# Optimization experiments

Hardware: AMD Instinct MI355X
Metric: run time of the kernel (lower is better)

Reference implementation:

```python
import jax, jax.numpy as jnp
import numpy as np

K = 4          # temporal_depth
IN_SIZE = 1024 # conv input channels
DN = ('NCDHW', 'OIDHW', 'NCDHW')


def setup_inputs() -> dict:
    key = jax.random.key(0)
    ks = jax.random.split(key, 12)
    B, T, C, H, W = 1, 8, IN_SIZE, 14, 14
    s = 0.02
    return {
        'videos': jax.random.normal(ks[0], (B, T, C, H, W), dtype=jnp.float32),
        # Conv3d(in_size, in_size, 3, padding='same')
        'conv1_w': jax.random.normal(ks[1], (IN_SIZE, IN_SIZE, 3, 3, 3), dtype=jnp.float32) * s,
        'conv1_b': jax.random.normal(ks[2], (IN_SIZE,), dtype=jnp.float32) * s,
        # Conv3d(in_size, 512, 3, padding='same')
        'conv2_w': jax.random.normal(ks[3], (512, IN_SIZE, 3, 3, 3), dtype=jnp.float32) * s,
        'conv2_b': jax.random.normal(ks[4], (512,), dtype=jnp.float32) * s,
        # Linear(512,512) -> Linear(512,512) -> Linear(512,128), torch (out,in) layout
        'l1_w': jax.random.normal(ks[5], (512, 512), dtype=jnp.float32) * s,
        'l1_b': jax.random.normal(ks[6], (512,), dtype=jnp.float32) * s,
        'l2_w': jax.random.normal(ks[7], (512, 512), dtype=jnp.float32) * s,
        'l2_b': jax.random.normal(ks[8], (512,), dtype=jnp.float32) * s,
        'l3_w': jax.random.normal(ks[9], (128, 512), dtype=jnp.float32) * s,
        'l3_b': jax.random.normal(ks[10], (128,), dtype=jnp.float32) * s,
    }


def reference(videos, conv1_w, conv1_b, conv2_w, conv2_b,
              l1_w, l1_b, l2_w, l2_b, l3_w, l3_b):
    B, T, C, H, W = videos.shape
    # prepend k zero frames, as in the torch code
    padded = jnp.concatenate(
        [jnp.zeros((B, K, C, H, W), videos.dtype), videos], axis=1)
    # window o covers padded frames [o, o+K) -> strictly-past original frames
    idx = jnp.arange(T)[:, None] + jnp.arange(K)[None, :]      # (T, K)
    win = padded[:, idx]                                        # (B, T, K, C, H, W)
    # permute(1,0,2,3): channels first, depth=K -> batch all windows together
    win = win.transpose(0, 1, 3, 2, 4, 5).reshape(B * T, C, K, H, W)
    # Conv3d + ReLU + Conv3d + ReLU, each with 'same' zero padding per window
    h = jax.lax.conv_general_dilated(win, conv1_w, (1, 1, 1), 'SAME',
                                     dimension_numbers=DN)
    h = jax.nn.relu(h + conv1_b[None, :, None, None, None])
    h = jax.lax.conv_general_dilated(h, conv2_w, (1, 1, 1), 'SAME',
                                     dimension_numbers=DN)
    h = jax.nn.relu(h + conv2_b[None, :, None, None, None])
    # MaxPool3d over the full (D,H,W) extent == global max per channel
    pooled = jnp.max(h, axis=(2, 3, 4))                         # (B*T, 512)
    x = jax.nn.relu(pooled @ l1_w.T + l1_b)
    x = jax.nn.relu(x @ l2_w.T + l2_b)
    x = jax.nn.relu(x @ l3_w.T + l3_b)                          # (B*T, 128)
    return x.reshape(B, T, 128)
```

## Files before the change

### kernel.cpp

```cpp
#include <hip/hip_runtime.h>

typedef __attribute__((ext_vector_type(8))) short short8;
typedef __attribute__((ext_vector_type(4))) int int4v;
typedef __attribute__((ext_vector_type(4))) float floatx4;
typedef __attribute__((ext_vector_type(4))) unsigned short ushort4v;

#define DEV __device__ __forceinline__

constexpr int M_TOT = 6272;
constexpr int M_PAD = 6400;

DEV void async_ld16(const void* g, void* l) {
  __builtin_amdgcn_global_load_lds(
      (const __attribute__((address_space(1))) unsigned int*)g,
      (__attribute__((address_space(3))) unsigned int*)l,
      16, 0, 0);
}

DEV unsigned short f2bf(float x) {
  union { float f; unsigned int u; } v; v.f = x;
  unsigned int u = v.u;
  u += 0x7FFFu + ((u >> 16) & 1u);
  return (unsigned short)(u >> 16);
}

DEV float bf2f(unsigned short s) {
  union { unsigned int u; float f; } v; v.u = ((unsigned int)s) << 16;
  return v.f;
}

__global__ void wtrans(const float* __restrict__ w, unsigned short* __restrict__ wt,
                       int total ) {
  __shared__ unsigned short l[256 * 27];
  const int tid  = threadIdx.x;
  const int base = blockIdx.x * 256;
  #pragma unroll 1
  for (int j = tid; j < 256 * 27; j += 256)
    l[j] = f2bf(w[(size_t)base * 27 + j]);
  __syncthreads();
  #pragma unroll 1
  for (int tap = 0; tap < 27; ++tap)
    wt[(size_t)tap * total + base + tid] = l[tid * 27 + tap];
}

__global__ void build_P1(const float* __restrict__ videos, unsigned short* __restrict__ P1) {
  const int f  = blockIdx.x;
  const int c0 = blockIdx.y * 64;
  const int tid = threadIdx.x;
  __shared__ unsigned short tile[64][196];

  #pragma unroll 1
  for (int it = 0; it < 49; ++it) {
    int idx = it * 256 + tid;
    int c = idx / 196, r = idx - c * 196;
    tile[c][r] = f2bf(videos[(size_t)(f * 1024 + c0 + c) * 196 + r]);
  }
  __syncthreads();

  const int c   = tid & 63;
  const int hwq = tid >> 6;
  #pragma unroll 1
  for (int s = 1; s <= 4; ++s) {
    int t = f + 5 - s;
    if (t > 7) continue;
    unsigned short* dst = P1 + (size_t)(t * 6 + s) * 256 * 1024 + (size_t)c0;
    #pragma unroll 1
    for (int it = 0; it < 49; ++it) {
      int hw = it * 4 + hwq;
      int h = hw / 14, w = hw - h * 14;
      dst[(size_t)((h + 1) * 16 + (w + 1)) * 1024 + c] = tile[c][hw];
    }
  }
}

#define DSR(dst, addr, off) \
  asm volatile("ds_read_b128 %0, %1 offset:" #off : "=&v"(dst) : "v"(addr))
#define WAITL(n) \
  asm volatile("s_waitcnt lgkmcnt(" #n ")" ::: "memory"); \
  __builtin_amdgcn_sched_barrier(0)
#define SB0 __builtin_amdgcn_sched_barrier(0)

template <int COUT, bool TCOND>
__global__ __launch_bounds__(512, 2) void conv_gemm(
    const unsigned short* __restrict__ P,
    const unsigned short* __restrict__ Wt,
    const unsigned int* __restrict__ sched,
    unsigned short* __restrict__ part)
{
  constexpr int CIN = 1024;
  __shared__ short lA[4][8192];
  __shared__ short lB[4][8192];
  const int tid  = threadIdx.x;
  const int wave = tid >> 6;
  const int lane = tid & 63;

  const unsigned int e = sched[blockIdx.x];
  const int x2   = e & 31;
  const int nidx = (e >> 5) & 3;
  const int zs   = (e >> 7) & 7;
  const int tap0 = (e >> 10) & 31;
  const int tap1 = (e >> 15) & 31;
  const int m0 = x2 * 256;
  const int n0 = nidx * 256;
  unsigned short* partOut = part + (size_t)zs * M_PAD * COUT;

  bool kdv[3] = {false, false, false};
  {
    const int cA = m0 / 196;
    int cB = (m0 + 255) / 196; if (cB > 31) cB = 31;
    for (int c = cA; c <= cB; ++c) {
      int t = c >> 2, d = c & 3;
      #pragma unroll
      for (int kd = 0; kd < 3; ++kd) {
        int s = d + kd;
        bool ok = (s >= 1) && (s <= 4);
        if (TCOND) ok = ok && (s >= 5 - t);
        kdv[kd] = kdv[kd] || ok;
      }
    }
  }

  const int arow = tid >> 2;
  const int aswz = (((tid & 3) ^ ((arow >> 1) & 3)) << 4);
  int aG[2], bG[2];
  #pragma unroll
  for (int q = 0; q < 2; ++q) {
    int m = m0 + q * 128 + arow;
    int t = m / 784;  int r2 = m - t * 784;
    int d = r2 / 196; int r3 = r2 - d * 196;
    int h = r3 / 14;  int w = r3 - h * 14;
    aG[q] = ((((t * 6 + d) * 16 + h) * 16 + w) * CIN) * 2 + aswz;
    bG[q] = (n0 + q * 128 + arow) * (CIN * 2) + aswz;
  }

  int nvt = 0;
  for (int tp = tap0; tp < tap1; ++tp) if (kdv[tp / 9]) ++nvt;
  const int steps = nvt * 32;
  int tap_s = tap0;
  while (tap_s < tap1 && !kdv[tap_s / 9]) ++tap_s;
  int c_s = 0;
  int stA = 0, stB = 0;
  auto setBases = [&]() {
    const int kd = tap_s / 9, rm = tap_s - kd * 9;
    const int kh = rm / 3, kw = rm - kh * 3;
    stA = ((((kd * 16) + kh) * 16 + kw) * CIN) * 2 + c_s * 2;
    stB = tap_s * (COUT * CIN * 2) + c_s * 2;
  };
  auto adv = [&]() {
    c_s += 32;
    if (c_s == CIN) { c_s = 0; do { ++tap_s; } while (tap_s < tap1 && !kdv[tap_s / 9]); }
  };

  const char* Pb = (const char*)P;
  const char* Wb = (const char*)Wt;
  char* lAc = (char*)&lA[0][0];
  char* lBc = (char*)&lB[0][0];
  const unsigned ldsA0 =
      (unsigned)(size_t)(__attribute__((address_space(3))) char*)lAc;
  const unsigned ldsB0 =
      (unsigned)(size_t)(__attribute__((address_space(3))) char*)lBc;

  #pragma unroll 1
  for (int s = 0; s < 3; ++s) {
    setBases();
    char* dA = lAc + s * 16384;
    char* dB = lBc + s * 16384;
    async_ld16(Pb + aG[0] + stA, dA + tid * 16);
    async_ld16(Wb + bG[0] + stB, dB + tid * 16);
    async_ld16(Pb + aG[1] + stA, dA + 8192 + tid * 16);
    async_ld16(Wb + bG[1] + stB, dB + 8192 + tid * 16);
    adv();
  }
  asm volatile("s_waitcnt vmcnt(4)" ::: "memory");
  __builtin_amdgcn_s_barrier();
  SB0;

  const int wm   = (wave >> 2) * 128;
  const int wn   = (wave & 3) * 64;
  const int quad = lane >> 4;
  const int l15  = lane & 15;
  const int segc = ((quad ^ ((l15 >> 1) & 3)) << 4);
  const unsigned rowA = ((unsigned)(wm + l15) << 6) + segc;
  const unsigned rowB = ((unsigned)(wn + l15) << 6) + segc;

  floatx4 acc[8][4];
  const floatx4 zero4 = {0.f, 0.f, 0.f, 0.f};
  #pragma unroll
  for (int i = 0; i < 8; ++i)
    #pragma unroll
    for (int j = 0; j < 4; ++j) acc[i][j] = zero4;

  int4v pbE0, pbE1, pbE2, pbE3, paE0, paE1;
  int4v pbO0, pbO1, pbO2, pbO3, paO0, paO1;

  {
    const unsigned aB = ldsA0 + rowA;
    const unsigned bB = ldsB0 + rowB;
    DSR(pbE0, bB, 0);
    DSR(pbE1, bB, 1024);
    DSR(pbE2, bB, 2048);
    DSR(pbE3, bB, 3072);
    DSR(paE0, aB, 0);
    DSR(paE1, aB, 1024);
  }
  SB0;

#define MFMA_GRP(ACCI, AV)                                                  \
  {                                                                         \
    short8 a_ = __builtin_bit_cast(short8, AV);                             \
    acc[ACCI][0] = __builtin_amdgcn_mfma_f32_16x16x32_bf16(a_, bs0, acc[ACCI][0], 0, 0, 0); \
    acc[ACCI][1] = __builtin_amdgcn_mfma_f32_16x16x32_bf16(a_, bs1, acc[ACCI][1], 0, 0, 0); \
    acc[ACCI][2] = __builtin_amdgcn_mfma_f32_16x16x32_bf16(a_, bs2, acc[ACCI][2], 0, 0, 0); \
    acc[ACCI][3] = __builtin_amdgcn_mfma_f32_16x16x32_bf16(a_, bs3, acc[ACCI][3], 0, 0, 0); \
  }

#define STEP_BODY(U, PB0, PB1, PB2, PB3, PA0, PA1, NB0, NB1, NB2, NB3, NA0, NA1) \
  {                                                                         \
    const int u_ = (U);                                                     \
    const bool h3s = (u_ + 3 < steps);                                      \
    const unsigned aB = ldsA0 + (unsigned)(u_ & 3) * 16384u + rowA;         \
    int4v f2, f3, f4, f5, f6, f7;                                           \
    DSR(f2, aB, 2048);                                                      \
    DSR(f3, aB, 3072);                                                      \
    DSR(f4, aB, 4096);                                                      \
    DSR(f5, aB, 5120);                                                      \
    DSR(f6, aB, 6144);                                                      \
    DSR(f7, aB, 7168);                                                      \
    SB0;                                                                    \
    if (h3s) {                                                              \
      setBases();                                                           \
      char* dA = lAc + ((u_ + 3) & 3) * 16384;                              \
      char* dB = lBc + ((u_ + 3) & 3) * 16384;                              \
      async_ld16(Pb + aG[0] + stA, dA + tid * 16);                          \
      async_ld16(Wb + bG[0] + stB, dB + tid * 16);                          \
      async_ld16(Pb + aG[1] + stA, dA + 8192 + tid * 16);                   \
      async_ld16(Wb + bG[1] + stB, dB + 8192 + tid * 16);                   \
      adv();                                                                \
    }                                                                       \
    SB0;                                                                    \
    __builtin_amdgcn_s_setprio(1);                                          \
    short8 bs0, bs1, bs2, bs3;                                              \
    WAITL(7);                                                               \
    bs0 = __builtin_bit_cast(short8, PB0);                                  \
    bs1 = __builtin_bit_cast(short8, PB1);                                  \
    bs2 = __builtin_bit_cast(short8, PB2);                                  \
    bs3 = __builtin_bit_cast(short8, PB3);                                  \
    MFMA_GRP(0, PA0);                                                       \
    WAITL(6); MFMA_GRP(1, PA1);                                             \
    WAITL(5); MFMA_GRP(2, f2);                                              \
    WAITL(4); MFMA_GRP(3, f3);                                              \
    WAITL(3); MFMA_GRP(4, f4);                                              \
    WAITL(2); MFMA_GRP(5, f5);                                              \
    WAITL(1); MFMA_GRP(6, f6);                                              \
    WAITL(0); MFMA_GRP(7, f7);                                              \
    __builtin_amdgcn_s_setprio(0);                                          \
    SB0;                                                                    \
    if (u_ + 1 < steps) {                                                   \
      const unsigned nA = ldsA0 + (unsigned)((u_ + 1) & 3) * 16384u + rowA; \
      const unsigned nB = ldsB0 + (unsigned)((u_ + 1) & 3) * 16384u + rowB; \
      DSR(NB0, nB, 0);                                                      \
      DSR(NB1, nB, 1024);                                                   \
      DSR(NB2, nB, 2048);                                                   \
      DSR(NB3, nB, 3072);                                                   \
      DSR(NA0, nA, 0);                                                      \
      DSR(NA1, nA, 1024);                                                   \
    }                                                                       \
    SB0;                                                                    \
    if (h3s) { asm volatile("s_waitcnt vmcnt(4)" ::: "memory"); }           \
    else     { asm volatile("s_waitcnt vmcnt(0)" ::: "memory"); }           \
    SB0;                                                                    \
    __builtin_amdgcn_s_barrier();                                           \
    SB0;                                                                    \
  }

  #pragma unroll 1
  for (int t = 0; t < steps; t += 2) {
    STEP_BODY(t,     pbE0, pbE1, pbE2, pbE3, paE0, paE1,
                     pbO0, pbO1, pbO2, pbO3, paO0, paO1);
    STEP_BODY(t + 1, pbO0, pbO1, pbO2, pbO3, paO0, paO1,
                     pbE0, pbE1, pbE2, pbE3, paE0, paE1);
  }

  asm volatile("s_waitcnt vmcnt(0) lgkmcnt(0)" ::: "memory");
  __builtin_amdgcn_s_barrier();

  #pragma unroll
  for (int j = 0; j < 4; ++j) {
    const int o = n0 + wn + j * 16 + l15;
    #pragma unroll
    for (int i = 0; i < 8; ++i) {
      #pragma unroll
      for (int r = 0; r < 4; ++r) {
        int m = m0 + wm + i * 16 + quad * 4 + r;
        partOut[(size_t)m * COUT + o] = f2bf(acc[i][j][r]);
      }
    }
  }
#undef STEP_BODY
#undef MFMA_GRP
}

__global__ void reduce_conv1(const unsigned short* __restrict__ part,
                             const float* __restrict__ bias,
                             unsigned short* __restrict__ P2) {
  const int idx = blockIdx.x * 256 + threadIdx.x;
  const int m  = idx >> 8;
  const int o4 = (idx & 255) * 4;
  const size_t ss = (size_t)M_PAD * 1024;
  const size_t base = (size_t)m * 1024 + o4;
  ushort4v p0 = *(const ushort4v*)(part + base);
  ushort4v p1 = *(const ushort4v*)(part + ss + base);
  ushort4v p2 = *(const ushort4v*)(part + 2 * ss + base);
  ushort4v out;
  #pragma unroll
  for (int k = 0; k < 4; ++k) {
    float v = bf2f(p0[k]) + bf2f(p1[k]) + bf2f(p2[k]) + bias[o4 + k];
    out[k] = f2bf(v > 0.f ? v : 0.f);
  }
  int t = m / 784;  int r2 = m - t * 784;
  int d = r2 / 196; int r3 = r2 - d * 196;
  int h = r3 / 14;  int w = r3 - h * 14;
  size_t didx = (size_t)(((t * 6 + d + 1) * 16 + (h + 1)) * 16 + (w + 1)) * 1024 + o4;
  *(ushort4v*)(P2 + didx) = out;
}

__global__ void reduce_conv2(const unsigned short* __restrict__ part,
                             const float* __restrict__ bias,
                             unsigned short* __restrict__ h2) {
  const int idx = blockIdx.x * 256 + threadIdx.x;
  const int m  = idx >> 7;
  const int o4 = (idx & 127) * 4;
  const size_t base = (size_t)m * 512 + o4;
  const size_t ss = (size_t)M_PAD * 512;
  float acc[4];
  #pragma unroll
  for (int k = 0; k < 4; ++k) acc[k] = bias[o4 + k];
  #pragma unroll
  for (int s = 0; s < 5; ++s) {
    ushort4v p = *(const ushort4v*)(part + (size_t)s * ss + base);
    #pragma unroll
    for (int k = 0; k < 4; ++k) acc[k] += bf2f(p[k]);
  }
  ushort4v out;
  #pragma unroll
  for (int k = 0; k < 4; ++k) out[k] = f2bf(acc[k] > 0.f ? acc[k] : 0.f);
  *(ushort4v*)(h2 + base) = out;
}

__global__ void pool1(const unsigned short* __restrict__ h2,
                      unsigned short* __restrict__ partial) {
  const int t = blockIdx.x / 28, ch = blockIdx.x % 28, o = threadIdx.x;
  const unsigned short* src = h2 + ((size_t)t * 784 + ch * 28) * 512 + o;
  unsigned short m = 0;
  #pragma unroll 4
  for (int i = 0; i < 28; ++i) { unsigned short v = src[(size_t)i * 512]; m = v > m ? v : m; }
  partial[((size_t)t * 28 + ch) * 512 + o] = m;
}

__global__ void pool2(const unsigned short* __restrict__ partial, float* __restrict__ pooled) {
  const int t = blockIdx.x, o = threadIdx.x;
  const unsigned short* src = partial + (size_t)t * 28 * 512 + o;
  unsigned short m = 0;
  #pragma unroll 4
  for (int i = 0; i < 28; ++i) { unsigned short v = src[(size_t)i * 512]; m = v > m ? v : m; }
  pooled[t * 512 + o] = bf2f(m);
}

__global__ void mlp_kernel(const float* __restrict__ pooled,
                           const float* __restrict__ w1, const float* __restrict__ b1,
                           const float* __restrict__ w2, const float* __restrict__ b2,
                           const float* __restrict__ w3, const float* __restrict__ b3,
                           float* __restrict__ out) {
  const int t = blockIdx.x, j = threadIdx.x;
  __shared__ float xa[512], xb[512];
  xa[j] = pooled[t * 512 + j];
  __syncthreads();
  {
    const float4* wr = (const float4*)(w1 + (size_t)j * 512);
    float s = b1[j];
    #pragma unroll 4
    for (int k = 0; k < 128; ++k) {
      float4 wv = wr[k];
      s += wv.x * xa[4*k] + wv.y * xa[4*k+1] + wv.z * xa[4*k+2] + wv.w * xa[4*k+3];
    }
    xb[j] = fmaxf(s, 0.f);
  }
  __syncthreads();
  {
    const float4* wr = (const float4*)(w2 + (size_t)j * 512);
    float s = b2[j];
    #pragma unroll 4
    for (int k = 0; k < 128; ++k) {
      float4 wv = wr[k];
      s += wv.x * xb[4*k] + wv.y * xb[4*k+1] + wv.z * xb[4*k+2] + wv.w * xb[4*k+3];
    }
    xa[j] = fmaxf(s, 0.f);
  }
  __syncthreads();
  if (j < 128) {
    const float4* wr = (const float4*)(w3 + (size_t)j * 512);
    float s = b3[j];
    #pragma unroll 4
    for (int k = 0; k < 128; ++k) {
      float4 wv = wr[k];
      s += wv.x * xa[4*k] + wv.y * xa[4*k+1] + wv.z * xa[4*k+2] + wv.w * xa[4*k+3];
    }
    out[t * 128 + j] = fmaxf(s, 0.f);
  }
}

static int build_sched(bool conv1, unsigned int* out) {
  const int nt = conv1 ? 4 : 2;
  unsigned int L[256];
  int cnt = 0;
  for (int n = 0; n < nt; ++n) {
    for (int x2 = 0; x2 < 25; ++x2) {
      const int m0 = x2 * 256;
      bool kdv[3] = {false, false, false};
      const int cA = m0 / 196;
      int cB = (m0 + 255) / 196; if (cB > 31) cB = 31;
      for (int c = cA; c <= cB; ++c) {
        int t = c >> 2, d = c & 3;
        for (int kd = 0; kd < 3; ++kd) {
          int s = d + kd;
          bool ok = (s >= 1 && s <= 4);
          if (conv1) ok = ok && (s >= 5 - t);
          kdv[kd] = kdv[kd] || ok;
        }
      }
      int vt[27], nv = 0;
      for (int tp = 0; tp < 27; ++tp) if (kdv[tp / 9]) vt[nv++] = tp;
      if (!nv) continue;
      const int ns = conv1 ? (nv / 9) : ((nv == 27) ? 5 : 4);
      for (int s = 0; s < ns; ++s) {
        int b0 = nv * s / ns, b1 = nv * (s + 1) / ns;
        int tp0 = vt[b0], tp1 = vt[b1 - 1] + 1;
        L[cnt++] = (unsigned int)(x2 | (n << 5) | (s << 7) | (tp0 << 10) | (tp1 << 15));
      }
    }
  }
  const int q = cnt / 8, r = cnt % 8;
  int pos = 0;
  for (int b = 0; b < 8; ++b) {
    const int nb = q + (b < r ? 1 : 0);
    for (int j = 0; j < nb; ++j) out[j * 8 + b] = L[pos++];
  }
  return cnt;
}

extern "C" void kernel_launch(void* const* d_in, const int* in_sizes, int n_in,
                              void* d_out, int out_size, void* d_ws, size_t ws_size,
                              hipStream_t stream) {
  const float* videos = (const float*)d_in[0];
  const float* c1w = (const float*)d_in[1];
  const float* c1b = (const float*)d_in[2];
  const float* c2w = (const float*)d_in[3];
  const float* c2b = (const float*)d_in[4];
  const float* l1w = (const float*)d_in[5];
  const float* l1b = (const float*)d_in[6];
  const float* l2w = (const float*)d_in[7];
  const float* l2b = (const float*)d_in[8];
  const float* l3w = (const float*)d_in[9];
  const float* l3b = (const float*)d_in[10];

  char* ws = (char*)d_ws;
  unsigned short* P12   = (unsigned short*)(ws);
  unsigned short* W1t   = (unsigned short*)(ws + 26738688);
  unsigned short* W2t   = (unsigned short*)(ws + 26738688);
  unsigned short* h2    = (unsigned short*)(ws + 55050240);
  float*          pooled= (float*)(ws + 61472768);
  unsigned short* ppart = (unsigned short*)(ws + 61489152);
  unsigned short* part  = (unsigned short*)(ws + 83361792);
  unsigned int* dsched1 = (unsigned int*)(ws + 122683392);
  unsigned int* dsched2 = (unsigned int*)(ws + 122684416);
  float* out = (float*)d_out;

  static unsigned int s1h[256], s2h[256];
  const int n1 = build_sched(true,  s1h);
  const int n2 = build_sched(false, s2h);
  hipMemcpyAsync(dsched1, s1h, sizeof(s1h), hipMemcpyHostToDevice, stream);
  hipMemcpyAsync(dsched2, s2h, sizeof(s2h), hipMemcpyHostToDevice, stream);

  hipMemsetAsync(ws, 0, 26738688, stream);
  hipMemsetAsync(part, 0, 39321600, stream);

  wtrans<<<4096, 256, 0, stream>>>(c1w, W1t, 1024 * 1024);
  build_P1<<<dim3(8, 16), 256, 0, stream>>>(videos, P12);

  conv_gemm<1024, true ><<<n1, 512, 0, stream>>>(P12, W1t, dsched1, part);

  wtrans<<<2048, 256, 0, stream>>>(c2w, W2t, 512 * 1024);
  reduce_conv1<<<6272, 256, 0, stream>>>(part, c1b, P12);
  hipMemsetAsync((char*)part + 32505856, 0, 262144, stream);

  conv_gemm<512, false><<<n2, 512, 0, stream>>>(P12, W2t, dsched2, part);
  reduce_conv2<<<3136, 256, 0, stream>>>(part, c2b, h2);

  pool1<<<224, 512, 0, stream>>>(h2, ppart);
  pool2<<<8, 512, 0, stream>>>(ppart, pooled);
  mlp_kernel<<<8, 512, 0, stream>>>(pooled, l1w, l1b, l2w, l2b, l3w, l3b, out);
}
```

Baseline: 748.0 us.

## Bake schedules into constant memory, drop memsets, fuse pool2 into MLP, simplify addressing

Schedules are computed at compile time into __constant__ tables, which removes two host-to-device copies and the host-side build each call. The 39MB zeroing of the partial buffer is dropped, and the reduce kernels now read only the split count that actually exists for each row tile. pool2 is folded into the MLP kernel, and the GEMM load addressing switches from recomputing offsets to incrementing pointers. The risk is that padded rows or splits that were never written could be read if a count table is wrong.

```diff
diff --git a/kernel.cpp b/kernel.cpp
--- a/kernel.cpp
+++ b/kernel.cpp
@@ -28,6 +28,73 @@
   union { unsigned int u; float f; } v; v.u = ((unsigned int)s) << 16;
   return v.f;
 }
+
+struct Sched { unsigned v[256]; int n; };
+struct NsTab { unsigned char v[25]; };
+
+constexpr void cell_kdv(bool conv1, int x2, bool kdv[3]) {
+  const int m0 = x2 * 256;
+  const int cA = m0 / 196;
+  int cB = (m0 + 255) / 196; if (cB > 31) cB = 31;
+  for (int c = cA; c <= cB; ++c) {
+    int t = c >> 2, d = c & 3;
+    for (int kd = 0; kd < 3; ++kd) {
+      int s = d + kd;
+      bool ok = (s >= 1 && s <= 4);
+      if (conv1) ok = ok && (s >= 5 - t);
+      kdv[kd] = kdv[kd] || ok;
+    }
+  }
+}
+
+constexpr Sched mk_sched(bool conv1) {
+  Sched out{};
+  const int nt = conv1 ? 4 : 2;
+  unsigned L[256] = {};
+  int cnt = 0;
+  for (int n = 0; n < nt; ++n) {
+    for (int x2 = 0; x2 < 25; ++x2) {
+      bool kdv[3] = {false, false, false};
+      cell_kdv(conv1, x2, kdv);
+      int vt[27] = {}; int nv = 0;
+      for (int tp = 0; tp < 27; ++tp) if (kdv[tp / 9]) vt[nv++] = tp;
+      if (!nv) continue;
+      const int ns = conv1 ? (nv / 9) : ((nv == 27) ? 5 : 4);
+      for (int s = 0; s < ns; ++s) {
+        int b0 = nv * s / ns, b1 = nv * (s + 1) / ns;
+        int tp0 = vt[b0], tp1 = vt[b1 - 1] + 1;
+        L[cnt++] = (unsigned)(x2 | (n << 5) | (s << 7) | (tp0 << 10) | (tp1 << 15));
+      }
+    }
+  }
+  const int q = cnt / 8, r = cnt % 8;
+  int pos = 0;
+  for (int b = 0; b < 8; ++b) {
+    const int nb = q + (b < r ? 1 : 0);
+    for (int j = 0; j < nb; ++j) out.v[j * 8 + b] = L[pos++];
+  }
+  out.n = cnt;
+  return out;
+}
+
+constexpr NsTab mk_ns(bool conv1) {
+  NsTab t{};
+  for (int x2 = 0; x2 < 25; ++x2) {
+    bool kdv[3] = {false, false, false};
+    cell_kdv(conv1, x2, kdv);
+    int nv = 0;
+    for (int tp = 0; tp < 27; ++tp) if (kdv[tp / 9]) ++nv;
+    t.v[x2] = (nv == 0) ? 0 : (unsigned char)(conv1 ? (nv / 9) : ((nv == 27) ? 5 : 4));
+  }
+  return t;
+}
+
+constexpr Sched S1h = mk_sched(true);
+constexpr Sched S2h = mk_sched(false);
+__constant__ Sched dS1 = mk_sched(true);
+__constant__ Sched dS2 = mk_sched(false);
+__constant__ NsTab dNS1 = mk_ns(true);
+__constant__ NsTab dNS2 = mk_ns(false);
 
 __global__ void wtrans(const float* __restrict__ w, unsigned short* __restrict__ wt,
                        int total ) {
@@ -84,7 +151,6 @@
 __global__ __launch_bounds__(512, 2) void conv_gemm(
     const unsigned short* __restrict__ P,
     const unsigned short* __restrict__ Wt,
-    const unsigned int* __restrict__ sched,
     unsigned short* __restrict__ part)
 {
   constexpr int CIN = 1024;
@@ -94,7 +160,7 @@
   const int wave = tid >> 6;
   const int lane = tid & 63;
 
-  const unsigned int e = sched[blockIdx.x];
+  const unsigned int e = (TCOND ? dS1 : dS2).v[blockIdx.x];
   const int x2   = e & 31;
   const int nidx = (e >> 5) & 3;
   const int zs   = (e >> 7) & 7;
@@ -136,23 +202,32 @@
   int nvt = 0;
   for (int tp = tap0; tp < tap1; ++tp) if (kdv[tp / 9]) ++nvt;
   const int steps = nvt * 32;
-  int tap_s = tap0;
-  while (tap_s < tap1 && !kdv[tap_s / 9]) ++tap_s;
-  int c_s = 0;
-  int stA = 0, stB = 0;
-  auto setBases = [&]() {
-    const int kd = tap_s / 9, rm = tap_s - kd * 9;
-    const int kh = rm / 3, kw = rm - kh * 3;
-    stA = ((((kd * 16) + kh) * 16 + kw) * CIN) * 2 + c_s * 2;
-    stB = tap_s * (COUT * CIN * 2) + c_s * 2;
-  };
-  auto adv = [&]() {
-    c_s += 32;
-    if (c_s == CIN) { c_s = 0; do { ++tap_s; } while (tap_s < tap1 && !kdv[tap_s / 9]); }
-  };
-
   const char* Pb = (const char*)P;
   const char* Wb = (const char*)Wt;
+
+  int tapS = tap0;
+  while (tapS < tap1 && !kdv[tapS / 9]) ++tapS;
+  int scnt = 0;
+  const char *pa0 = nullptr, *pa1 = nullptr, *pb0 = nullptr, *pb1 = nullptr;
+  auto tapBase = [&]() {
+    const int kd = tapS / 9, rm = tapS - kd * 9;
+    const int kh = rm / 3, kw = rm - kh * 3;
+    const int tA = ((((kd * 16) + kh) * 16 + kw) * CIN) * 2;
+    const int tB = tapS * (COUT * CIN * 2);
+    pa0 = Pb + aG[0] + tA;  pa1 = Pb + aG[1] + tA;
+    pb0 = Wb + bG[0] + tB;  pb1 = Wb + bG[1] + tB;
+  };
+  auto advS = [&]() {
+    if (++scnt == 32) {
+      scnt = 0;
+      do { ++tapS; } while (tapS < tap1 && !kdv[tapS / 9]);
+      if (tapS < tap1) tapBase();
+    } else {
+      pa0 += 64; pa1 += 64; pb0 += 64; pb1 += 64;
+    }
+  };
+  tapBase();
+
   char* lAc = (char*)&lA[0][0];
   char* lBc = (char*)&lB[0][0];
   const unsigned ldsA0 =
@@ -162,14 +237,13 @@
 
   #pragma unroll 1
   for (int s = 0; s < 3; ++s) {
-    setBases();
     char* dA = lAc + s * 16384;
     char* dB = lBc + s * 16384;
-    async_ld16(Pb + aG[0] + stA, dA + tid * 16);
-    async_ld16(Wb + bG[0] + stB, dB + tid * 16);
-    async_ld16(Pb + aG[1] + stA, dA + 8192 + tid * 16);
-    async_ld16(Wb + bG[1] + stB, dB + 8192 + tid * 16);
-    adv();
+    async_ld16(pa0, dA + tid * 16);
+    async_ld16(pb0, dB + tid * 16);
+    async_ld16(pa1, dA + 8192 + tid * 16);
+    async_ld16(pb1, dB + 8192 + tid * 16);
+    advS();
   }
   asm volatile("s_waitcnt vmcnt(4)" ::: "memory");
   __builtin_amdgcn_s_barrier();
@@ -228,14 +302,13 @@
     DSR(f7, aB, 7168);                                                      \
     SB0;                                                                    \
     if (h3s) {                                                              \
-      setBases();                                                           \
       char* dA = lAc + ((u_ + 3) & 3) * 16384;                              \
       char* dB = lBc + ((u_ + 3) & 3) * 16384;                              \
-      async_ld16(Pb + aG[0] + stA, dA + tid * 16);                          \
-      async_ld16(Wb + bG[0] + stB, dB + tid * 16);                          \
-      async_ld16(Pb + aG[1] + stA, dA + 8192 + tid * 16);                   \
-      async_ld16(Wb + bG[1] + stB, dB + 8192 + tid * 16);                   \
-      adv();                                                                \
+      async_ld16(pa0, dA + tid * 16);                                       \
+      async_ld16(pb0, dB + tid * 16);                                       \
+      async_ld16(pa1, dA + 8192 + tid * 16);                                \
+      async_ld16(pb1, dB + 8192 + tid * 16);                                \
+      advS();                                                               \
     }                                                                       \
     SB0;                                                                    \
     __builtin_amdgcn_s_setprio(1);                                          \
@@ -303,20 +376,23 @@
 __global__ void reduce_conv1(const unsigned short* __restrict__ part,
                              const float* __restrict__ bias,
                              unsigned short* __restrict__ P2) {
-  const int idx = blockIdx.x * 256 + threadIdx.x;
-  const int m  = idx >> 8;
-  const int o4 = (idx & 255) * 4;
+  const int m  = blockIdx.x;
+  const int o4 = threadIdx.x * 4;
+  const int ns = dNS1.v[m >> 8];
   const size_t ss = (size_t)M_PAD * 1024;
   const size_t base = (size_t)m * 1024 + o4;
-  ushort4v p0 = *(const ushort4v*)(part + base);
-  ushort4v p1 = *(const ushort4v*)(part + ss + base);
-  ushort4v p2 = *(const ushort4v*)(part + 2 * ss + base);
+  float v[4];
+  #pragma unroll
+  for (int k = 0; k < 4; ++k) v[k] = bias[o4 + k];
+  #pragma unroll 1
+  for (int z = 0; z < ns; ++z) {
+    ushort4v p = *(const ushort4v*)(part + (size_t)z * ss + base);
+    #pragma unroll
+    for (int k = 0; k < 4; ++k) v[k] += bf2f(p[k]);
+  }
   ushort4v out;
   #pragma unroll
-  for (int k = 0; k < 4; ++k) {
-    float v = bf2f(p0[k]) + bf2f(p1[k]) + bf2f(p2[k]) + bias[o4 + k];
-    out[k] = f2bf(v > 0.f ? v : 0.f);
-  }
+  for (int k = 0; k < 4; ++k) out[k] = f2bf(v[k] > 0.f ? v[k] : 0.f);
   int t = m / 784;  int r2 = m - t * 784;
   int d = r2 / 196; int r3 = r2 - d * 196;
   int h = r3 / 14;  int w = r3 - h * 14;
@@ -330,13 +406,14 @@
   const int idx = blockIdx.x * 256 + threadIdx.x;
   const int m  = idx >> 7;
   const int o4 = (idx & 127) * 4;
+  const int ns = dNS2.v[m >> 8];
   const size_t base = (size_t)m * 512 + o4;
   const size_t ss = (size_t)M_PAD * 512;
   float acc[4];
   #pragma unroll
   for (int k = 0; k < 4; ++k) acc[k] = bias[o4 + k];
-  #pragma unroll
-  for (int s = 0; s < 5; ++s) {
+  #pragma unroll 1
+  for (int s = 0; s < ns; ++s) {
     ushort4v p = *(const ushort4v*)(part + (size_t)s * ss + base);
     #pragma unroll
     for (int k = 0; k < 4; ++k) acc[k] += bf2f(p[k]);
@@ -357,23 +434,20 @@
   partial[((size_t)t * 28 + ch) * 512 + o] = m;
 }
 
-__global__ void pool2(const unsigned short* __restrict__ partial, float* __restrict__ pooled) {
-  const int t = blockIdx.x, o = threadIdx.x;
-  const unsigned short* src = partial + (size_t)t * 28 * 512 + o;
-  unsigned short m = 0;
-  #pragma unroll 4
-  for (int i = 0; i < 28; ++i) { unsigned short v = src[(size_t)i * 512]; m = v > m ? v : m; }
-  pooled[t * 512 + o] = bf2f(m);
-}
-
-__global__ void mlp_kernel(const float* __restrict__ pooled,
+__global__ void mlp_kernel(const unsigned short* __restrict__ ppart,
                            const float* __restrict__ w1, const float* __restrict__ b1,
                            const float* __restrict__ w2, const float* __restrict__ b2,
                            const float* __restrict__ w3, const float* __restrict__ b3,
                            float* __restrict__ out) {
   const int t = blockIdx.x, j = threadIdx.x;
   __shared__ float xa[512], xb[512];
-  xa[j] = pooled[t * 512 + j];
+  {
+    const unsigned short* src = ppart + (size_t)t * 28 * 512 + j;
+    unsigned short m = 0;
+    #pragma unroll 4
+    for (int i = 0; i < 28; ++i) { unsigned short v = src[(size_t)i * 512]; m = v > m ? v : m; }
+    xa[j] = bf2f(m);
+  }
   __syncthreads();
   {
     const float4* wr = (const float4*)(w1 + (size_t)j * 512);
@@ -407,45 +481,6 @@
     }
     out[t * 128 + j] = fmaxf(s, 0.f);
   }
-}
-
-static int build_sched(bool conv1, unsigned int* out) {
-  const int nt = conv1 ? 4 : 2;
-  unsigned int L[256];
-  int cnt = 0;
-  for (int n = 0; n < nt; ++n) {
-    for (int x2 = 0; x2 < 25; ++x2) {
-      const int m0 = x2 * 256;
-      bool kdv[3] = {false, false, false};
-      const int cA = m0 / 196;
-      int cB = (m0 + 255) / 196; if (cB > 31) cB = 31;
-      for (int c = cA; c <= cB; ++c) {
-        int t = c >> 2, d = c & 3;
-        for (int kd = 0; kd < 3; ++kd) {
-          int s = d + kd;
-          bool ok = (s >= 1 && s <= 4);
-          if (conv1) ok = ok && (s >= 5 - t);
-          kdv[kd] = kdv[kd] || ok;
-        }
-      }
-      int vt[27], nv = 0;
-      for (int tp = 0; tp < 27; ++tp) if (kdv[tp / 9]) vt[nv++] = tp;
-      if (!nv) continue;
-      const int ns = conv1 ? (nv / 9) : ((nv == 27) ? 5 : 4);
-      for (int s = 0; s < ns; ++s) {
-        int b0 = nv * s / ns, b1 = nv * (s + 1) / ns;
-        int tp0 = vt[b0], tp1 = vt[b1 - 1] + 1;
-        L[cnt++] = (unsigned int)(x2 | (n << 5) | (s << 7) | (tp0 << 10) | (tp1 << 15));
-      }
-    }
-  }
-  const int q = cnt / 8, r = cnt % 8;
-  int pos = 0;
-  for (int b = 0; b < 8; ++b) {
-    const int nb = q + (b < r ? 1 : 0);
-    for (int j = 0; j < nb; ++j) out[j * 8 + b] = L[pos++];
-  }
-  return cnt;
 }
 
 extern "C" void kernel_launch(void* const* d_in, const int* in_sizes, int n_in,
@@ -468,35 +503,23 @@
   unsigned short* W1t   = (unsigned short*)(ws + 26738688);
   unsigned short* W2t   = (unsigned short*)(ws + 26738688);
   unsigned short* h2    = (unsigned short*)(ws + 55050240);
-  float*          pooled= (float*)(ws + 61472768);
   unsigned short* ppart = (unsigned short*)(ws + 61489152);
   unsigned short* part  = (unsigned short*)(ws + 83361792);
-  unsigned int* dsched1 = (unsigned int*)(ws + 122683392);
-  unsigned int* dsched2 = (unsigned int*)(ws + 122684416);
   float* out = (float*)d_out;
 
-  static unsigned int s1h[256], s2h[256];
-  const int n1 = build_sched(true,  s1h);
-  const int n2 = build_sched(false, s2h);
-  hipMemcpyAsync(dsched1, s1h, sizeof(s1h), hipMemcpyHostToDevice, stream);
-  hipMemcpyAsync(dsched2, s2h, sizeof(s2h), hipMemcpyHostToDevice, stream);
-
   hipMemsetAsync(ws, 0, 26738688, stream);
-  hipMemsetAsync(part, 0, 39321600, stream);
 
   wtrans<<<4096, 256, 0, stream>>>(c1w, W1t, 1024 * 1024);
   build_P1<<<dim3(8, 16), 256, 0, stream>>>(videos, P12);
 
-  conv_gemm<1024, true ><<<n1, 512, 0, stream>>>(P12, W1t, dsched1, part);
+  conv_gemm<1024, true ><<<S1h.n, 512, 0, stream>>>(P12, W1t, part);
 
   wtrans<<<2048, 256, 0, stream>>>(c2w, W2t, 512 * 1024);
   reduce_conv1<<<6272, 256, 0, stream>>>(part, c1b, P12);
-  hipMemsetAsync((char*)part + 32505856, 0, 262144, stream);
-
-  conv_gemm<512, false><<<n2, 512, 0, stream>>>(P12, W2t, dsched2, part);
+
+  conv_gemm<512, false><<<S2h.n, 512, 0, stream>>>(P12, W2t, part);
   reduce_conv2<<<3136, 256, 0, stream>>>(part, c2b, h2);
 
   pool1<<<224, 512, 0, stream>>>(h2, ppart);
-  pool2<<<8, 512, 0, stream>>>(ppart, pooled);
-  mlp_kernel<<<8, 512, 0, stream>>>(pooled, l1w, l1b, l2w, l2b, l3w, l3b, out);
-}
+  mlp_kernel<<<8, 512, 0, stream>>>(ppart, l1w, l1b, l2w, l2b, l3w, l3b, out);
+}
```

After: 746.1 us. No clear change (-0.3%).
